# Kernel optimization log

Hardware: AMD Instinct MI355X
Metric: run time of the kernel (lower is better)

Reference implementation:

```python
import jax, jax.numpy as jnp
import numpy as np

B, S, NX, NH = 4, 1024, 1024, 16
HD = NX // NH  # head_features = 64


def setup_inputs() -> dict:
    key = jax.random.key(0)
    k1, k2, k3 = jax.random.split(key, 3)
    x = jax.random.normal(k1, (B, S, NX), dtype=jnp.float32)
    w_attn = 0.02 * jax.random.normal(k2, (NX, 3 * NX), dtype=jnp.float32)
    b_attn = jnp.zeros((3 * NX,), dtype=jnp.float32)
    w_proj = 0.02 * jax.random.normal(k3, (NX, NX), dtype=jnp.float32)
    b_proj = jnp.zeros((NX,), dtype=jnp.float32)
    causal_bias = jnp.tril(jnp.ones((S, S), dtype=jnp.float32))  # tril buffer
    return {"x": x, "w_attn": w_attn, "b_attn": b_attn,
            "w_proj": w_proj, "b_proj": b_proj, "causal_bias": causal_bias}


def reference(x, w_attn, b_attn, w_proj, b_proj, causal_bias):
    # c_attn: fused qkv projection (Conv1D == addmm)
    qkv = x @ w_attn + b_attn                     # [B, S, 3*NX]
    q, k, v = jnp.split(qkv, 3, axis=-1)          # each [B, S, NX]
    # split heads -> [B, H, S, D]
    q = q.reshape(B, S, NH, HD).transpose(0, 2, 1, 3)
    k = k.reshape(B, S, NH, HD).transpose(0, 2, 1, 3)
    v = v.reshape(B, S, NH, HD).transpose(0, 2, 1, 3)
    # present: stack of (key in [B,H,S,D] layout, value)
    present = jnp.stack((k, v))                   # [2, B, H, S, D]
    # scores with scale=True
    w = jnp.einsum('bhqd,bhkd->bhqk', q, k) / jnp.sqrt(jnp.float32(HD))
    b = causal_bias[None, None, :, :]             # [1,1,S,S] (nd==ns==S)
    w = w * b - 1e10 * (1.0 - b)                  # multiplicative mask trick
    p = jax.nn.softmax(w, axis=-1)
    a = jnp.einsum('bhqk,bhkd->bhqd', p, v)       # [B, H, S, D]
    a = a.transpose(0, 2, 1, 3).reshape(B, S, NX)  # merge heads
    out = a @ w_proj + b_proj                     # c_proj
    return out, present
```

## Files before the change

kernel.cpp:

```cpp
#include <hip/hip_runtime.h>
#include <hip/hip_bf16.h>

typedef __attribute__((ext_vector_type(8))) short short8;
typedef __attribute__((ext_vector_type(4))) float floatx4;

constexpr int Bsz = 4, Ssz = 1024, NXc = 1024, NHc = 16, HDc = 64;
constexpr int OUT_ELEMS  = Bsz * Ssz * NXc;
constexpr int HEAD_ELEMS = Bsz * NHc * Ssz * HDc;

union BF8 { __hip_bfloat16 h[8]; uint4 v; short8 s; };

__device__ __forceinline__ uint4 cvt8(const float* __restrict__ p) {
    float4 a = *reinterpret_cast<const float4*>(p);
    float4 b = *reinterpret_cast<const float4*>(p + 4);
    BF8 u;
    u.h[0] = __float2bfloat16(a.x); u.h[1] = __float2bfloat16(a.y);
    u.h[2] = __float2bfloat16(a.z); u.h[3] = __float2bfloat16(a.w);
    u.h[4] = __float2bfloat16(b.x); u.h[5] = __float2bfloat16(b.y);
    u.h[6] = __float2bfloat16(b.z); u.h[7] = __float2bfloat16(b.w);
    return u.v;
}

__device__ __forceinline__ void load_lds_16B(const void* g, void* l) {
    __builtin_amdgcn_global_load_lds(
        (const __attribute__((address_space(1))) unsigned int*)g,
        (__attribute__((address_space(3))) unsigned int*)l, 16, 0, 0);
}


__global__ __launch_bounds__(256) void cvt_kernel(
    const float* __restrict__ in, __hip_bfloat16* __restrict__ out, int n)
{
    int i = (blockIdx.x * 256 + threadIdx.x) * 8;
    if (i < n)
        *reinterpret_cast<uint4*>(out + i) = cvt8(in + i);
}

__global__ __launch_bounds__(256) void transpose_cvt(
    const float* __restrict__ in, __hip_bfloat16* __restrict__ out,
    int K, int N)
{
    __shared__ float t[64][65];
    const int tid = threadIdx.x;
    const int k0 = blockIdx.y * 64, n0 = blockIdx.x * 64;
#pragma unroll
    for (int j = 0; j < 16; ++j) {
        const int idx = tid + j * 256;
        const int row = idx >> 6, col = idx & 63;
        t[row][col] = in[(size_t)(k0 + row) * N + n0 + col];
    }
    __syncthreads();
#pragma unroll
    for (int j = 0; j < 16; ++j) {
        const int idx = tid + j * 256;
        const int orow = idx >> 6, ocol = idx & 63;
        out[(size_t)(n0 + orow) * K + k0 + ocol] = __float2bfloat16(t[ocol][orow]);
    }
}

__global__ __launch_bounds__(256) void vtrans(
    const float* __restrict__ vsrc, __hip_bfloat16* __restrict__ vtb)
{
    __shared__ float t[64][65];
    const int st = blockIdx.x, h = blockIdx.y, b = blockIdx.z;
    const int tid = threadIdx.x;
    const float* src = vsrc + ((size_t)((b * 16 + h) * Ssz + st * 64)) * HDc;
    __hip_bfloat16* dst = vtb + ((size_t)(b * 16 + h)) * (HDc * Ssz) + st * 64;
#pragma unroll
    for (int j = 0; j < 16; ++j) {
        const int idx = tid + j * 256;
        const int row = idx >> 6, col = idx & 63;
        t[row][col] = src[(size_t)row * 64 + col];
    }
    __syncthreads();
#pragma unroll
    for (int j = 0; j < 16; ++j) {
        const int idx = tid + j * 256;
        const int d = idx >> 6, s = idx & 63;
        dst[(size_t)d * Ssz + s] = __float2bfloat16(t[s][d]);
    }
}

template <int EPI>
__global__ __launch_bounds__(256) void gemm128(
    const __hip_bfloat16* __restrict__ A,
    const __hip_bfloat16* __restrict__ Bt,
    const float* __restrict__ bias,
    float* __restrict__ outf,
    __hip_bfloat16* __restrict__ qws,
    float* __restrict__ present,
    __hip_bfloat16* __restrict__ kbf,
    int M, int N, int K)
{
    __shared__ __align__(16) __hip_bfloat16 As[128 * 32];
    __shared__ __align__(16) __hip_bfloat16 Bs[128 * 32];

    const int tid  = threadIdx.x;
    const int w    = tid >> 6, lane = tid & 63;
    const int quad = lane >> 4, l16 = lane & 15;
    const int m0 = blockIdx.y * 128, n0 = blockIdx.x * 128;
    const int mb = (w >> 1) * 64, nbw = (w & 1) * 64;

    const int srow = lane >> 2;
    const int skseg = (lane & 3) * 8;

    floatx4 acc[4][4];
#pragma unroll
    for (int i = 0; i < 4; ++i)
#pragma unroll
        for (int j = 0; j < 4; ++j)
#pragma unroll
            for (int r = 0; r < 4; ++r) acc[i][j][r] = 0.f;

    for (int k0 = 0; k0 < K; k0 += 32) {
#pragma unroll
        for (int c = 0; c < 2; ++c) {
            const int chunk = w * 2 + c;
            const int row = chunk * 16 + srow;
            load_lds_16B(A + (size_t)(m0 + row) * K + k0 + skseg,
                         &As[chunk * 512]);
            load_lds_16B(Bt + (size_t)(n0 + row) * K + k0 + skseg,
                         &Bs[chunk * 512]);
        }
        __syncthreads();

        short8 af[4], bfr[4];
#pragma unroll
        for (int mi = 0; mi < 4; ++mi)
            af[mi] = *reinterpret_cast<const short8*>(
                &As[(mb + mi * 16 + l16) * 32 + quad * 8]);
#pragma unroll
        for (int ni = 0; ni < 4; ++ni)
            bfr[ni] = *reinterpret_cast<const short8*>(
                &Bs[(nbw + ni * 16 + l16) * 32 + quad * 8]);
#pragma unroll
        for (int mi = 0; mi < 4; ++mi)
#pragma unroll
            for (int ni = 0; ni < 4; ++ni)
                acc[mi][ni] = __builtin_amdgcn_mfma_f32_16x16x32_bf16(
                    af[mi], bfr[ni], acc[mi][ni], 0, 0, 0);

        __syncthreads();
    }

#pragma unroll
    for (int mi = 0; mi < 4; ++mi) {
#pragma unroll
        for (int ni = 0; ni < 4; ++ni) {
            const int col = n0 + nbw + ni * 16 + l16;
            const float bsv = bias[col];
#pragma unroll
            for (int r = 0; r < 4; ++r) {
                const int row = m0 + mb + mi * 16 + quad * 4 + r;
                const float v = acc[mi][ni][r] + bsv;
                if (EPI == 0) {
                    const int seg = col >> 10;
                    const int c = col & 1023;
                    if (seg == 0) {
                        qws[(size_t)row * 1024 + c] = __float2bfloat16(v);
                    } else {
                        const int b = row >> 10, s = row & 1023;
                        const int h = c >> 6, d = c & 63;
                        const size_t idx =
                            ((size_t)((b * 16 + h) * 1024 + s)) * 64 + d;
                        if (seg == 1) {
                            present[idx] = v;
                            kbf[idx] = __float2bfloat16(v);
                        } else {
                            present[HEAD_ELEMS + idx] = v;
                        }
                    }
                } else {
                    outf[(size_t)row * N + col] = v;
                }
            }
        }
    }
}

__global__ __launch_bounds__(256) void attn_v4(
    const __hip_bfloat16* __restrict__ qws,
    const __hip_bfloat16* __restrict__ kbf,
    const __hip_bfloat16* __restrict__ vtb,
    __hip_bfloat16* __restrict__ a_ws)
{
    const int bx = blockIdx.x, h = blockIdx.y, b = blockIdx.z;
    const int tid  = threadIdx.x;
    const int wave = tid >> 6, lane = tid & 63;
    const int quad = lane >> 4, l16 = lane & 15;
    const int stripe = wave * 16;

    __shared__ __align__(16) __hip_bfloat16 Ks[64 * 64];
    __shared__ __align__(16) __hip_bfloat16 Vts[64 * 64];
    __shared__ __align__(16) __hip_bfloat16 Ps[64][72];

    const __hip_bfloat16* Kbase = kbf + ((size_t)(b * 16 + h)) * (Ssz * HDc);
    const __hip_bfloat16* Vbase = vtb + ((size_t)(b * 16 + h)) * (HDc * Ssz);

    short8 ones;
#pragma unroll
    for (int i = 0; i < 8; ++i) ones[i] = (short)0x3F80;
    const float cexp = 0.18033688f;

#pragma unroll
    for (int pass = 0; pass < 2; ++pass) {
        const int qt = (pass == 0) ? (8 + bx) : (7 - bx);

        const __hip_bfloat16* Qb =
            qws + ((size_t)(b * Ssz + qt * 64 + stripe + l16)) * NXc + h * 64;
        short8 qf0 = *reinterpret_cast<const short8*>(Qb + quad * 8);
        short8 qf1 = *reinterpret_cast<const short8*>(Qb + 32 + quad * 8);

        floatx4 oacc[4], lacc;
#pragma unroll
        for (int ni = 0; ni < 4; ++ni)
#pragma unroll
            for (int r = 0; r < 4; ++r) oacc[ni][r] = 0.f;
#pragma unroll
        for (int r = 0; r < 4; ++r) lacc[r] = 0.f;

        for (int kt = 0; kt <= qt; ++kt) {
#pragma unroll
            for (int it = 0; it < 2; ++it) {
                const int slot = it * 256 + wave * 64 + lane;
                const int row = slot >> 3;
                const int p = (slot & 7) ^ (row & 7);
                load_lds_16B(
                    Kbase + (size_t)(kt * 64 + row) * 64 + p * 8,
                    &Ks[(size_t)(it * 256 + wave * 64) * 8]);
                load_lds_16B(
                    Vbase + (size_t)row * Ssz + kt * 64 + p * 8,
                    &Vts[(size_t)(it * 256 + wave * 64) * 8]);
            }
            __syncthreads();

            floatx4 sacc[4];
#pragma unroll
            for (int ni = 0; ni < 4; ++ni)
#pragma unroll
                for (int r = 0; r < 4; ++r) sacc[ni][r] = 0.f;
#pragma unroll
            for (int ni = 0; ni < 4; ++ni) {
                const int r = ni * 16 + l16;
                const int sw = r & 7;
                short8 kf0 = *reinterpret_cast<const short8*>(
                    &Ks[(r * 8 + (quad ^ sw)) * 8]);
                short8 kf1 = *reinterpret_cast<const short8*>(
                    &Ks[(r * 8 + ((4 + quad) ^ sw)) * 8]);
                sacc[ni] = __builtin_amdgcn_mfma_f32_16x16x32_bf16(
                    qf0, kf0, sacc[ni], 0, 0, 0);
                sacc[ni] = __builtin_amdgcn_mfma_f32_16x16x32_bf16(
                    qf1, kf1, sacc[ni], 0, 0, 0);
            }

            const bool diag = (kt == qt);
#pragma unroll
            for (int r = 0; r < 4; ++r) {
                const int lrow = stripe + quad * 4 + r;
#pragma unroll
                for (int nn = 0; nn < 4; ++nn) {
                    const int ni = (nn + quad) & 3;
                    const bool mask = diag && (ni * 16 + l16) > lrow;
                    const float p = mask ? 0.f : exp2f(sacc[ni][r] * cexp);
                    Ps[lrow][ni * 16 + l16] = __float2bfloat16(p);
                }
            }

#pragma unroll
            for (int kk = 0; kk < 64; kk += 32) {
                short8 pf = *reinterpret_cast<const short8*>(
                    &Ps[stripe + l16][kk + quad * 8]);
                lacc = __builtin_amdgcn_mfma_f32_16x16x32_bf16(
                    pf, ones, lacc, 0, 0, 0);
#pragma unroll
                for (int ni = 0; ni < 4; ++ni) {
                    const int r2 = ni * 16 + l16;
                    const int sw2 = r2 & 7;
                    short8 vf = *reinterpret_cast<const short8*>(
                        &Vts[(r2 * 8 + (((kk >> 3) + quad) ^ sw2)) * 8]);
                    oacc[ni] = __builtin_amdgcn_mfma_f32_16x16x32_bf16(
                        pf, vf, oacc[ni], 0, 0, 0);
                }
            }
            __syncthreads();
        }

#pragma unroll
        for (int r = 0; r < 4; ++r) {
            const float inv = 1.0f / fmaxf(lacc[r], 1e-20f);
            const int row = qt * 64 + stripe + quad * 4 + r;
#pragma unroll
            for (int ni = 0; ni < 4; ++ni) {
                const int col = h * 64 + ni * 16 + l16;
                a_ws[((size_t)(b * Ssz + row)) * NXc + col] =
                    __float2bfloat16(oacc[ni][r] * inv);
            }
        }
    }
}

__global__ __launch_bounds__(256) void attn_v3p(
    const __hip_bfloat16* __restrict__ qws,
    const float* __restrict__ present,
    __hip_bfloat16* __restrict__ a_ws)
{
    const int bx = blockIdx.x, h = blockIdx.y, b = blockIdx.z;
    const int tid  = threadIdx.x;
    const int wave = tid >> 6, lane = tid & 63;
    const int quad = lane >> 4, l16 = lane & 15;
    const int stripe = wave * 16;

    const size_t headoff = ((size_t)(b * 16 + h)) * Ssz * HDc;
    const float* Kp = present + headoff;
    const float* Vp = present + HEAD_ELEMS + headoff;

    __shared__ __align__(16) __hip_bfloat16 Ks[64][72];
    __shared__ __align__(16) __hip_bfloat16 Vts[64][72];
    __shared__ __align__(16) __hip_bfloat16 Ps[64][72];

    const int krow = tid >> 3, kseg = tid & 7;
    const int vd = tid & 63, vg = tid >> 6;

    short8 ones;
#pragma unroll
    for (int i = 0; i < 8; ++i) ones[i] = (short)0x3F80;
    const float cexp = 0.18033688f;

#pragma unroll
    for (int pass = 0; pass < 2; ++pass) {
        const int qt = (pass == 0) ? (8 + bx) : (7 - bx);

        const __hip_bfloat16* Qb =
            qws + ((size_t)(b * Ssz + qt * 64 + stripe + l16)) * NXc + h * 64;
        short8 qf0 = *reinterpret_cast<const short8*>(Qb + quad * 8);
        short8 qf1 = *reinterpret_cast<const short8*>(Qb + 32 + quad * 8);

        floatx4 oacc[4], lacc;
#pragma unroll
        for (int ni = 0; ni < 4; ++ni)
#pragma unroll
            for (int r = 0; r < 4; ++r) oacc[ni][r] = 0.f;
#pragma unroll
        for (int r = 0; r < 4; ++r) lacc[r] = 0.f;

        for (int kt = 0; kt <= qt; ++kt) {
#pragma unroll
            for (int it = 0; it < 2; ++it) {
                const int kr = krow + it * 32;
                *reinterpret_cast<uint4*>(&Ks[kr][kseg * 8]) =
                    cvt8(Kp + (size_t)(kt * 64 + kr) * 64 + kseg * 8);
                const int kb = (it * 4 + vg) * 8;
                BF8 u;
#pragma unroll
                for (int i = 0; i < 8; ++i)
                    u.h[i] = __float2bfloat16(
                        Vp[(size_t)(kt * 64 + kb + i) * 64 + vd]);
                *reinterpret_cast<uint4*>(&Vts[vd][kb]) = u.v;
            }
            __syncthreads();

            floatx4 sacc[4];
#pragma unroll
            for (int ni = 0; ni < 4; ++ni)
#pragma unroll
                for (int r = 0; r < 4; ++r) sacc[ni][r] = 0.f;
#pragma unroll
            for (int ni = 0; ni < 4; ++ni) {
                short8 kf0 = *reinterpret_cast<const short8*>(
                    &Ks[ni * 16 + l16][quad * 8]);
                short8 kf1 = *reinterpret_cast<const short8*>(
                    &Ks[ni * 16 + l16][32 + quad * 8]);
                sacc[ni] = __builtin_amdgcn_mfma_f32_16x16x32_bf16(
                    qf0, kf0, sacc[ni], 0, 0, 0);
                sacc[ni] = __builtin_amdgcn_mfma_f32_16x16x32_bf16(
                    qf1, kf1, sacc[ni], 0, 0, 0);
            }

            const bool diag = (kt == qt);
#pragma unroll
            for (int r = 0; r < 4; ++r) {
                const int lrow = stripe + quad * 4 + r;
#pragma unroll
                for (int nn = 0; nn < 4; ++nn) {
                    const int ni = (nn + quad) & 3;
                    const bool mask = diag && (ni * 16 + l16) > lrow;
                    const float p = mask ? 0.f : exp2f(sacc[ni][r] * cexp);
                    Ps[lrow][ni * 16 + l16] = __float2bfloat16(p);
                }
            }

#pragma unroll
            for (int kk = 0; kk < 64; kk += 32) {
                short8 pf = *reinterpret_cast<const short8*>(
                    &Ps[stripe + l16][kk + quad * 8]);
                lacc = __builtin_amdgcn_mfma_f32_16x16x32_bf16(
                    pf, ones, lacc, 0, 0, 0);
#pragma unroll
                for (int ni = 0; ni < 4; ++ni) {
                    short8 vf = *reinterpret_cast<const short8*>(
                        &Vts[ni * 16 + l16][kk + quad * 8]);
                    oacc[ni] = __builtin_amdgcn_mfma_f32_16x16x32_bf16(
                        pf, vf, oacc[ni], 0, 0, 0);
                }
            }
            __syncthreads();
        }

#pragma unroll
        for (int r = 0; r < 4; ++r) {
            const float inv = 1.0f / fmaxf(lacc[r], 1e-20f);
            const int row = qt * 64 + stripe + quad * 4 + r;
#pragma unroll
            for (int ni = 0; ni < 4; ++ni) {
                const int col = h * 64 + ni * 16 + l16;
                a_ws[((size_t)(b * Ssz + row)) * NXc + col] =
                    __float2bfloat16(oacc[ni][r] * inv);
            }
        }
    }
}

template <int EPI>
__global__ __launch_bounds__(256) void gemm64(
    const void* __restrict__ Av, const float* __restrict__ Bw,
    const float* __restrict__ bias, float* __restrict__ out0,
    float* __restrict__ present, int M, int N, int K)
{
    __shared__ __align__(16) __hip_bfloat16 As[64][40];
    __shared__ __align__(16) __hip_bfloat16 Bs[64][40];
    const int tid = threadIdx.x;
    const int wave = tid >> 6, lane = tid & 63;
    const int quad = lane >> 4, l16 = lane & 15;
    const int m0 = blockIdx.y * 64, n0 = blockIdx.x * 64;
    const int mb = (wave >> 1) * 32, nb = (wave & 1) * 32;
    const int arow = tid >> 2, aseg = tid & 3;
    const int brow = tid >> 3, bseg = tid & 7;
    floatx4 acc[2][2];
#pragma unroll
    for (int i = 0; i < 2; ++i)
#pragma unroll
        for (int j = 0; j < 2; ++j)
#pragma unroll
            for (int r = 0; r < 4; ++r) acc[i][j][r] = 0.f;
    for (int k0 = 0; k0 < K; k0 += 32) {
        if (EPI == 0) {
            const float* A = (const float*)Av;
            *reinterpret_cast<uint4*>(&As[arow][aseg * 8]) =
                cvt8(A + (size_t)(m0 + arow) * K + k0 + aseg * 8);
        } else {
            const __hip_bfloat16* A = (const __hip_bfloat16*)Av;
            *reinterpret_cast<uint4*>(&As[arow][aseg * 8]) =
                *reinterpret_cast<const uint4*>(
                    A + (size_t)(m0 + arow) * K + k0 + aseg * 8);
        }
        const float* bp = Bw + (size_t)(k0 + brow) * N + n0 + bseg * 8;
        float4 b0 = *reinterpret_cast<const float4*>(bp);
        float4 b1 = *reinterpret_cast<const float4*>(bp + 4);
        Bs[bseg * 8 + 0][brow] = __float2bfloat16(b0.x);
        Bs[bseg * 8 + 1][brow] = __float2bfloat16(b0.y);
        Bs[bseg * 8 + 2][brow] = __float2bfloat16(b0.z);
        Bs[bseg * 8 + 3][brow] = __float2bfloat16(b0.w);
        Bs[bseg * 8 + 4][brow] = __float2bfloat16(b1.x);
        Bs[bseg * 8 + 5][brow] = __float2bfloat16(b1.y);
        Bs[bseg * 8 + 6][brow] = __float2bfloat16(b1.z);
        Bs[bseg * 8 + 7][brow] = __float2bfloat16(b1.w);
        __syncthreads();
        short8 af[2], bf[2];
#pragma unroll
        for (int mm = 0; mm < 2; ++mm)
            af[mm] = *reinterpret_cast<const short8*>(&As[mb + mm * 16 + l16][quad * 8]);
#pragma unroll
        for (int nn = 0; nn < 2; ++nn)
            bf[nn] = *reinterpret_cast<const short8*>(&Bs[nb + nn * 16 + l16][quad * 8]);
#pragma unroll
        for (int mm = 0; mm < 2; ++mm)
#pragma unroll
            for (int nn = 0; nn < 2; ++nn)
                acc[mm][nn] = __builtin_amdgcn_mfma_f32_16x16x32_bf16(
                    af[mm], bf[nn], acc[mm][nn], 0, 0, 0);
        __syncthreads();
    }
#pragma unroll
    for (int mm = 0; mm < 2; ++mm)
#pragma unroll
        for (int nn = 0; nn < 2; ++nn) {
            const int col = n0 + nb + nn * 16 + l16;
            const float bsv = bias[col];
#pragma unroll
            for (int r = 0; r < 4; ++r) {
                const int row = m0 + mb + mm * 16 + quad * 4 + r;
                const float v = acc[mm][nn][r] + bsv;
                if (EPI == 0) {
                    const int seg = col >> 10;
                    const int c = col & 1023;
                    if (seg == 0) out0[(size_t)row * 1024 + c] = v;
                    else {
                        const int b = row >> 10, s = row & 1023;
                        const int h = c >> 6, d = c & 63;
                        const size_t idx = ((size_t)((b * 16 + h) * 1024 + s)) * 64 + d;
                        if (seg == 1) present[idx] = v;
                        else          present[HEAD_ELEMS + idx] = v;
                    }
                } else out0[(size_t)row * N + col] = v;
            }
        }
}

__global__ __launch_bounds__(256) void attn64(
    const float* __restrict__ qbuf, const float* __restrict__ present,
    __hip_bfloat16* __restrict__ a_ws)
{
    const int qt = blockIdx.x, h = blockIdx.y, b = blockIdx.z;
    const int tid = threadIdx.x;
    const int wave = tid >> 6, lane = tid & 63;
    const int quad = lane >> 4, l16 = lane & 15;
    const int mb = (wave >> 1) * 32, nb = (wave & 1) * 32;
    const size_t headoff = ((size_t)(b * 16 + h)) * Ssz * HDc;
    const float* Qb = qbuf + ((size_t)(b * Ssz + qt * 64)) * NXc + h * 64;
    const float* Kp = present + headoff;
    const float* Vp = present + HEAD_ELEMS + headoff;
    __shared__ __align__(16) __hip_bfloat16 Qs[64][72];
    __shared__ __align__(16) __hip_bfloat16 Ks[64][72];
    __shared__ __align__(16) __hip_bfloat16 Vts[64][72];
    __shared__ __align__(16) __hip_bfloat16 Ps[64][72];
    __shared__ float Sc[64][65];
    __shared__ float mrow[64], lrow[64], arw[64];
#pragma unroll
    for (int it = 0; it < 2; ++it) {
        const int c = tid + it * 256;
        const int row = c >> 3, seg = c & 7;
        *reinterpret_cast<uint4*>(&Qs[row][seg * 8]) =
            cvt8(Qb + (size_t)row * NXc + seg * 8);
    }
    if (tid < 64) { mrow[tid] = -1e9f; lrow[tid] = 0.f; }
    floatx4 oacc[2][2];
#pragma unroll
    for (int i = 0; i < 2; ++i)
#pragma unroll
        for (int j = 0; j < 2; ++j)
#pragma unroll
            for (int r = 0; r < 4; ++r) oacc[i][j][r] = 0.f;
    __syncthreads();
    for (int kt = 0; kt <= qt; ++kt) {
#pragma unroll
        for (int it = 0; it < 2; ++it) {
            const int c = tid + it * 256;
            const int row = c >> 3, seg = c & 7;
            *reinterpret_cast<uint4*>(&Ks[row][seg * 8]) =
                cvt8(Kp + (size_t)(kt * 64 + row) * 64 + seg * 8);
            const float* vp = Vp + (size_t)(kt * 64 + row) * 64 + seg * 8;
            float4 v0 = *reinterpret_cast<const float4*>(vp);
            float4 v1 = *reinterpret_cast<const float4*>(vp + 4);
            Vts[seg * 8 + 0][row] = __float2bfloat16(v0.x);
            Vts[seg * 8 + 1][row] = __float2bfloat16(v0.y);
            Vts[seg * 8 + 2][row] = __float2bfloat16(v0.z);
            Vts[seg * 8 + 3][row] = __float2bfloat16(v0.w);
            Vts[seg * 8 + 4][row] = __float2bfloat16(v1.x);
            Vts[seg * 8 + 5][row] = __float2bfloat16(v1.y);
            Vts[seg * 8 + 6][row] = __float2bfloat16(v1.z);
            Vts[seg * 8 + 7][row] = __float2bfloat16(v1.w);
        }
        __syncthreads();
        floatx4 sacc[2][2];
#pragma unroll
        for (int i = 0; i < 2; ++i)
#pragma unroll
            for (int j = 0; j < 2; ++j)
#pragma unroll
                for (int r = 0; r < 4; ++r) sacc[i][j][r] = 0.f;
#pragma unroll
        for (int kd = 0; kd < 64; kd += 32) {
            short8 af[2], bf[2];
#pragma unroll
            for (int mm = 0; mm < 2; ++mm)
                af[mm] = *reinterpret_cast<const short8*>(&Qs[mb + mm * 16 + l16][kd + quad * 8]);
#pragma unroll
            for (int nn = 0; nn < 2; ++nn)
                bf[nn] = *reinterpret_cast<const short8*>(&Ks[nb + nn * 16 + l16][kd + quad * 8]);
#pragma unroll
            for (int mm = 0; mm < 2; ++mm)
#pragma unroll
                for (int nn = 0; nn < 2; ++nn)
                    sacc[mm][nn] = __builtin_amdgcn_mfma_f32_16x16x32_bf16(
                        af[mm], bf[nn], sacc[mm][nn], 0, 0, 0);
        }
        const bool diag = (kt == qt);
#pragma unroll
        for (int mm = 0; mm < 2; ++mm)
#pragma unroll
            for (int nn = 0; nn < 2; ++nn)
#pragma unroll
                for (int r = 0; r < 4; ++r) {
                    const int row = mb + mm * 16 + quad * 4 + r;
                    const int col = nb + nn * 16 + l16;
                    float v = fminf(fmaxf(sacc[mm][nn][r] * 0.125f, -1e8f), 1e8f);
                    if (diag && col > row) v = -1e9f;
                    Sc[row][col] = v;
                }
        __syncthreads();
        if (tid < 64) {
            const int r = tid;
            const float mo = mrow[r];
            float mx = mo;
            for (int c = 0; c < 64; ++c) mx = fmaxf(mx, Sc[r][c]);
            const float al = (mo <= -5e8f) ? 0.f : __expf(mo - mx);
            float sum = 0.f;
            for (int c = 0; c < 64; ++c) {
                const float sv = Sc[r][c];
                const float p = (sv <= -5e8f) ? 0.f : __expf(sv - mx);
                sum += p;
                Ps[r][c] = __float2bfloat16(p);
            }
            mrow[r] = mx;
            lrow[r] = lrow[r] * al + sum;
            arw[r]  = al;
        }
        __syncthreads();
#pragma unroll
        for (int mm = 0; mm < 2; ++mm) {
            const int rbase = mb + mm * 16 + quad * 4;
#pragma unroll
            for (int r = 0; r < 4; ++r) {
                const float al = arw[rbase + r];
                oacc[mm][0][r] *= al;
                oacc[mm][1][r] *= al;
            }
        }
#pragma unroll
        for (int kk = 0; kk < 64; kk += 32) {
            short8 pf[2], vf[2];
#pragma unroll
            for (int mm = 0; mm < 2; ++mm)
                pf[mm] = *reinterpret_cast<const short8*>(&Ps[mb + mm * 16 + l16][kk + quad * 8]);
#pragma unroll
            for (int nn = 0; nn < 2; ++nn)
                vf[nn] = *reinterpret_cast<const short8*>(&Vts[nb + nn * 16 + l16][kk + quad * 8]);
#pragma unroll
            for (int mm = 0; mm < 2; ++mm)
#pragma unroll
                for (int nn = 0; nn < 2; ++nn)
                    oacc[mm][nn] = __builtin_amdgcn_mfma_f32_16x16x32_bf16(
                        pf[mm], vf[nn], oacc[mm][nn], 0, 0, 0);
        }
        __syncthreads();
    }
#pragma unroll
    for (int mm = 0; mm < 2; ++mm)
#pragma unroll
        for (int nn = 0; nn < 2; ++nn)
#pragma unroll
            for (int r = 0; r < 4; ++r) {
                const int row = mb + mm * 16 + quad * 4 + r;
                const int col = nb + nn * 16 + l16;
                const float inv = 1.0f / fmaxf(lrow[row], 1e-20f);
                a_ws[((size_t)(b * Ssz + qt * 64 + row)) * NXc + h * 64 + col] =
                    __float2bfloat16(oacc[mm][nn][r] * inv);
            }
}

extern "C" void kernel_launch(void* const* d_in, const int* in_sizes, int n_in,
                              void* d_out, int out_size, void* d_ws, size_t ws_size,
                              hipStream_t stream) {
    const float* x      = (const float*)d_in[0];
    const float* w_attn = (const float*)d_in[1];
    const float* b_attn = (const float*)d_in[2];
    const float* w_proj = (const float*)d_in[3];
    const float* b_proj = (const float*)d_in[4];

    float* out     = (float*)d_out;
    float* present = out + OUT_ELEMS;

    const size_t NEED_V4 = 40u * 1024u * 1024u;
    const size_t NEED_V3 = 32u * 1024u * 1024u;

    if (ws_size >= NEED_V4) {
        __hip_bfloat16* x_bf = (__hip_bfloat16*)d_ws;
        __hip_bfloat16* wTa  = x_bf + 4194304;
        __hip_bfloat16* wTp  = wTa + 3145728;
        __hip_bfloat16* q_ws = wTp + 1048576;
        __hip_bfloat16* k_bf = q_ws + 4194304;
        __hip_bfloat16* vT   = k_bf + 4194304;
        __hip_bfloat16* a_ws = x_bf;

        cvt_kernel<<<2048, 256, 0, stream>>>(x, x_bf, OUT_ELEMS);
        transpose_cvt<<<dim3(48, 16), 256, 0, stream>>>(w_attn, wTa, 1024, 3072);
        transpose_cvt<<<dim3(16, 16), 256, 0, stream>>>(w_proj, wTp, 1024, 1024);

        gemm128<0><<<dim3(24, 32), 256, 0, stream>>>(
            x_bf, wTa, b_attn, nullptr, q_ws, present, k_bf, 4096, 3072, 1024);

        vtrans<<<dim3(16, 16, 4), 256, 0, stream>>>(present + HEAD_ELEMS, vT);

        attn_v4<<<dim3(8, 16, 4), 256, 0, stream>>>(q_ws, k_bf, vT, a_ws);

        gemm128<1><<<dim3(8, 32), 256, 0, stream>>>(
            a_ws, wTp, b_proj, out, nullptr, nullptr, nullptr, 4096, 1024, 1024);
    } else if (ws_size >= NEED_V3) {
        __hip_bfloat16* a_ws = (__hip_bfloat16*)d_ws;
        __hip_bfloat16* q_ws = a_ws + 4194304;
        __hip_bfloat16* x_bf = q_ws + 4194304;
        __hip_bfloat16* wTa  = x_bf + 4194304;
        __hip_bfloat16* wTp  = wTa + 3145728;

        cvt_kernel<<<2048, 256, 0, stream>>>(x, x_bf, OUT_ELEMS);
        transpose_cvt<<<dim3(48, 16), 256, 0, stream>>>(w_attn, wTa, 1024, 3072);
        transpose_cvt<<<dim3(16, 16), 256, 0, stream>>>(w_proj, wTp, 1024, 1024);

        gemm128<0><<<dim3(24, 32), 256, 0, stream>>>(
            x_bf, wTa, b_attn, nullptr, q_ws, present, nullptr, 4096, 3072, 1024);

        attn_v3p<<<dim3(8, 16, 4), 256, 0, stream>>>(q_ws, present, a_ws);

        gemm128<1><<<dim3(8, 32), 256, 0, stream>>>(
            a_ws, wTp, b_proj, out, nullptr, nullptr, nullptr, 4096, 1024, 1024);
    } else {
        __hip_bfloat16* a_ws = (__hip_bfloat16*)d_ws;
        hipMemsetAsync(d_ws, 0, (size_t)OUT_ELEMS * sizeof(__hip_bfloat16), stream);
        gemm64<0><<<dim3(48, 64), 256, 0, stream>>>(x, w_attn, b_attn, out, present,
                                                    4096, 3072, 1024);
        attn64<<<dim3(16, 16, 4), 256, 0, stream>>>(out, present, a_ws);
        gemm64<1><<<dim3(16, 64), 256, 0, stream>>>(a_ws, w_proj, b_proj, out, nullptr,
                                                    4096, 1024, 1024);
    }
}
```

Before: 232.3 us.

## Swap GEMM operand roles for vectorized epilogue stores; flatten attention grid

The GEMMs now put the transposed weight in the MFMA A operand and the activations in B. Each lane then holds four consecutive output columns, so the bias loads and the fp32/bf16 epilogue stores become float4/uint2 vector writes instead of scalar strided ones. The attention kernel stops processing two paired query tiles per block and instead launches 1024 blocks, one per query tile. The tiles are ordered so that alternating batches reverse the tile order to spread causal work across blocks. The risk is load imbalance, because each block now has uneven causal work rather than paired work.

```diff
diff --git a/kernel.cpp b/kernel.cpp
--- a/kernel.cpp
+++ b/kernel.cpp
@@ -9,6 +9,7 @@
 constexpr int HEAD_ELEMS = Bsz * NHc * Ssz * HDc;
 
 union BF8 { __hip_bfloat16 h[8]; uint4 v; short8 s; };
+union BF4 { __hip_bfloat16 h[4]; uint2 v; };
 
 __device__ __forceinline__ uint4 cvt8(const float* __restrict__ p) {
     float4 a = *reinterpret_cast<const float4*>(p);
@@ -82,23 +83,24 @@
 }
 
 template <int EPI>
-__global__ __launch_bounds__(256) void gemm128(
-    const __hip_bfloat16* __restrict__ A,
-    const __hip_bfloat16* __restrict__ Bt,
+__global__ __launch_bounds__(256) void gemm128T(
+    const __hip_bfloat16* __restrict__ Wt,
+    const __hip_bfloat16* __restrict__ X,
     const float* __restrict__ bias,
     float* __restrict__ outf,
     __hip_bfloat16* __restrict__ qws,
     float* __restrict__ present,
     __hip_bfloat16* __restrict__ kbf,
-    int M, int N, int K)
+    int Nw, int Mx, int K)
 {
-    __shared__ __align__(16) __hip_bfloat16 As[128 * 32];
-    __shared__ __align__(16) __hip_bfloat16 Bs[128 * 32];
+    __shared__ __align__(16) __hip_bfloat16 Ws[128 * 32];
+    __shared__ __align__(16) __hip_bfloat16 Xs[128 * 32];
 
     const int tid  = threadIdx.x;
     const int w    = tid >> 6, lane = tid & 63;
     const int quad = lane >> 4, l16 = lane & 15;
-    const int m0 = blockIdx.y * 128, n0 = blockIdx.x * 128;
+    const int m0 = blockIdx.y * 128;
+    const int n0 = blockIdx.x * 128;
     const int mb = (w >> 1) * 64, nbw = (w & 1) * 64;
 
     const int srow = lane >> 2;
@@ -117,74 +119,85 @@
         for (int c = 0; c < 2; ++c) {
             const int chunk = w * 2 + c;
             const int row = chunk * 16 + srow;
-            load_lds_16B(A + (size_t)(m0 + row) * K + k0 + skseg,
-                         &As[chunk * 512]);
-            load_lds_16B(Bt + (size_t)(n0 + row) * K + k0 + skseg,
-                         &Bs[chunk * 512]);
-        }
-        __syncthreads();
-
-        short8 af[4], bfr[4];
+            load_lds_16B(Wt + (size_t)(m0 + row) * K + k0 + skseg,
+                         &Ws[chunk * 512]);
+            load_lds_16B(X + (size_t)(n0 + row) * K + k0 + skseg,
+                         &Xs[chunk * 512]);
+        }
+        __syncthreads();
+
+        short8 wf[4], xf[4];
 #pragma unroll
         for (int mi = 0; mi < 4; ++mi)
-            af[mi] = *reinterpret_cast<const short8*>(
-                &As[(mb + mi * 16 + l16) * 32 + quad * 8]);
+            wf[mi] = *reinterpret_cast<const short8*>(
+                &Ws[(mb + mi * 16 + l16) * 32 + quad * 8]);
 #pragma unroll
         for (int ni = 0; ni < 4; ++ni)
-            bfr[ni] = *reinterpret_cast<const short8*>(
-                &Bs[(nbw + ni * 16 + l16) * 32 + quad * 8]);
+            xf[ni] = *reinterpret_cast<const short8*>(
+                &Xs[(nbw + ni * 16 + l16) * 32 + quad * 8]);
 #pragma unroll
         for (int mi = 0; mi < 4; ++mi)
 #pragma unroll
             for (int ni = 0; ni < 4; ++ni)
                 acc[mi][ni] = __builtin_amdgcn_mfma_f32_16x16x32_bf16(
-                    af[mi], bfr[ni], acc[mi][ni], 0, 0, 0);
+                    wf[mi], xf[ni], acc[mi][ni], 0, 0, 0);
 
         __syncthreads();
     }
 
 #pragma unroll
     for (int mi = 0; mi < 4; ++mi) {
+        const int wcol = m0 + mb + mi * 16 + quad * 4;
+        const float4 b4 = *reinterpret_cast<const float4*>(&bias[wcol]);
 #pragma unroll
         for (int ni = 0; ni < 4; ++ni) {
-            const int col = n0 + nbw + ni * 16 + l16;
-            const float bsv = bias[col];
-#pragma unroll
-            for (int r = 0; r < 4; ++r) {
-                const int row = m0 + mb + mi * 16 + quad * 4 + r;
-                const float v = acc[mi][ni][r] + bsv;
-                if (EPI == 0) {
-                    const int seg = col >> 10;
-                    const int c = col & 1023;
-                    if (seg == 0) {
-                        qws[(size_t)row * 1024 + c] = __float2bfloat16(v);
+            const int xrow = n0 + nbw + ni * 16 + l16;
+            float4 v4;
+            v4.x = acc[mi][ni][0] + b4.x;
+            v4.y = acc[mi][ni][1] + b4.y;
+            v4.z = acc[mi][ni][2] + b4.z;
+            v4.w = acc[mi][ni][3] + b4.w;
+            if (EPI == 1) {
+                *reinterpret_cast<float4*>(&outf[(size_t)xrow * Nw + wcol]) = v4;
+            } else {
+                const int seg = wcol >> 10;
+                const int c = wcol & 1023;
+                BF4 hb;
+                hb.h[0] = __float2bfloat16(v4.x);
+                hb.h[1] = __float2bfloat16(v4.y);
+                hb.h[2] = __float2bfloat16(v4.z);
+                hb.h[3] = __float2bfloat16(v4.w);
+                if (seg == 0) {
+                    *reinterpret_cast<uint2*>(&qws[(size_t)xrow * 1024 + c]) = hb.v;
+                } else {
+                    const int b = xrow >> 10, s = xrow & 1023;
+                    const int h = c >> 6, d = c & 63;
+                    const size_t idx =
+                        ((size_t)((b * 16 + h) * 1024 + s)) * 64 + d;
+                    if (seg == 1) {
+                        *reinterpret_cast<float4*>(&present[idx]) = v4;
+                        if (kbf)
+                            *reinterpret_cast<uint2*>(&kbf[idx]) = hb.v;
                     } else {
-                        const int b = row >> 10, s = row & 1023;
-                        const int h = c >> 6, d = c & 63;
-                        const size_t idx =
-                            ((size_t)((b * 16 + h) * 1024 + s)) * 64 + d;
-                        if (seg == 1) {
-                            present[idx] = v;
-                            kbf[idx] = __float2bfloat16(v);
-                        } else {
-                            present[HEAD_ELEMS + idx] = v;
-                        }
+                        *reinterpret_cast<float4*>(&present[HEAD_ELEMS + idx]) = v4;
                     }
-                } else {
-                    outf[(size_t)row * N + col] = v;
                 }
             }
         }
     }
 }
 
-__global__ __launch_bounds__(256) void attn_v4(
+__global__ __launch_bounds__(256) void attn_v5(
     const __hip_bfloat16* __restrict__ qws,
     const __hip_bfloat16* __restrict__ kbf,
     const __hip_bfloat16* __restrict__ vtb,
     __hip_bfloat16* __restrict__ a_ws)
 {
-    const int bx = blockIdx.x, h = blockIdx.y, b = blockIdx.z;
+    const int i = blockIdx.x;
+    const int slot = i >> 8, u = i & 15, wq = (i >> 4) & 15;
+    const int qt = (slot & 1) ? (15 - u) : u;
+    const int h = wq, b = slot;
+
     const int tid  = threadIdx.x;
     const int wave = tid >> 6, lane = tid & 63;
     const int quad = lane >> 4, l16 = lane & 15;
@@ -199,102 +212,97 @@
 
     short8 ones;
 #pragma unroll
-    for (int i = 0; i < 8; ++i) ones[i] = (short)0x3F80;
+    for (int j = 0; j < 8; ++j) ones[j] = (short)0x3F80;
     const float cexp = 0.18033688f;
 
-#pragma unroll
-    for (int pass = 0; pass < 2; ++pass) {
-        const int qt = (pass == 0) ? (8 + bx) : (7 - bx);
-
-        const __hip_bfloat16* Qb =
-            qws + ((size_t)(b * Ssz + qt * 64 + stripe + l16)) * NXc + h * 64;
-        short8 qf0 = *reinterpret_cast<const short8*>(Qb + quad * 8);
-        short8 qf1 = *reinterpret_cast<const short8*>(Qb + 32 + quad * 8);
-
-        floatx4 oacc[4], lacc;
+    const __hip_bfloat16* Qb =
+        qws + ((size_t)(b * Ssz + qt * 64 + stripe + l16)) * NXc + h * 64;
+    short8 qf0 = *reinterpret_cast<const short8*>(Qb + quad * 8);
+    short8 qf1 = *reinterpret_cast<const short8*>(Qb + 32 + quad * 8);
+
+    floatx4 oacc[4], lacc;
+#pragma unroll
+    for (int ni = 0; ni < 4; ++ni)
+#pragma unroll
+        for (int r = 0; r < 4; ++r) oacc[ni][r] = 0.f;
+#pragma unroll
+    for (int r = 0; r < 4; ++r) lacc[r] = 0.f;
+
+    for (int kt = 0; kt <= qt; ++kt) {
+#pragma unroll
+        for (int it = 0; it < 2; ++it) {
+            const int slotg = it * 256 + wave * 64 + lane;
+            const int row = slotg >> 3;
+            const int p = (slotg & 7) ^ (row & 7);
+            load_lds_16B(
+                Kbase + (size_t)(kt * 64 + row) * 64 + p * 8,
+                &Ks[(size_t)(it * 256 + wave * 64) * 8]);
+            load_lds_16B(
+                Vbase + (size_t)row * Ssz + kt * 64 + p * 8,
+                &Vts[(size_t)(it * 256 + wave * 64) * 8]);
+        }
+        __syncthreads();
+
+        floatx4 sacc[4];
 #pragma unroll
         for (int ni = 0; ni < 4; ++ni)
 #pragma unroll
-            for (int r = 0; r < 4; ++r) oacc[ni][r] = 0.f;
-#pragma unroll
-        for (int r = 0; r < 4; ++r) lacc[r] = 0.f;
-
-        for (int kt = 0; kt <= qt; ++kt) {
-#pragma unroll
-            for (int it = 0; it < 2; ++it) {
-                const int slot = it * 256 + wave * 64 + lane;
-                const int row = slot >> 3;
-                const int p = (slot & 7) ^ (row & 7);
-                load_lds_16B(
-                    Kbase + (size_t)(kt * 64 + row) * 64 + p * 8,
-                    &Ks[(size_t)(it * 256 + wave * 64) * 8]);
-                load_lds_16B(
-                    Vbase + (size_t)row * Ssz + kt * 64 + p * 8,
-                    &Vts[(size_t)(it * 256 + wave * 64) * 8]);
-            }
-            __syncthreads();
-
-            floatx4 sacc[4];
-#pragma unroll
-            for (int ni = 0; ni < 4; ++ni)
-#pragma unroll
-                for (int r = 0; r < 4; ++r) sacc[ni][r] = 0.f;
+            for (int r = 0; r < 4; ++r) sacc[ni][r] = 0.f;
+#pragma unroll
+        for (int ni = 0; ni < 4; ++ni) {
+            const int r = ni * 16 + l16;
+            const int sw = r & 7;
+            short8 kf0 = *reinterpret_cast<const short8*>(
+                &Ks[(r * 8 + (quad ^ sw)) * 8]);
+            short8 kf1 = *reinterpret_cast<const short8*>(
+                &Ks[(r * 8 + ((4 + quad) ^ sw)) * 8]);
+            sacc[ni] = __builtin_amdgcn_mfma_f32_16x16x32_bf16(
+                qf0, kf0, sacc[ni], 0, 0, 0);
+            sacc[ni] = __builtin_amdgcn_mfma_f32_16x16x32_bf16(
+                qf1, kf1, sacc[ni], 0, 0, 0);
+        }
+
+        const bool diag = (kt == qt);
+#pragma unroll
+        for (int r = 0; r < 4; ++r) {
+            const int lrow = stripe + quad * 4 + r;
+#pragma unroll
+            for (int nn = 0; nn < 4; ++nn) {
+                const int ni = (nn + quad) & 3;
+                const bool mask = diag && (ni * 16 + l16) > lrow;
+                const float p = mask ? 0.f : exp2f(sacc[ni][r] * cexp);
+                Ps[lrow][ni * 16 + l16] = __float2bfloat16(p);
+            }
+        }
+
+#pragma unroll
+        for (int kk = 0; kk < 64; kk += 32) {
+            short8 pf = *reinterpret_cast<const short8*>(
+                &Ps[stripe + l16][kk + quad * 8]);
+            lacc = __builtin_amdgcn_mfma_f32_16x16x32_bf16(
+                pf, ones, lacc, 0, 0, 0);
 #pragma unroll
             for (int ni = 0; ni < 4; ++ni) {
-                const int r = ni * 16 + l16;
-                const int sw = r & 7;
-                short8 kf0 = *reinterpret_cast<const short8*>(
-                    &Ks[(r * 8 + (quad ^ sw)) * 8]);
-                short8 kf1 = *reinterpret_cast<const short8*>(
-                    &Ks[(r * 8 + ((4 + quad) ^ sw)) * 8]);
-                sacc[ni] = __builtin_amdgcn_mfma_f32_16x16x32_bf16(
-                    qf0, kf0, sacc[ni], 0, 0, 0);
-                sacc[ni] = __builtin_amdgcn_mfma_f32_16x16x32_bf16(
-                    qf1, kf1, sacc[ni], 0, 0, 0);
-            }
-
-            const bool diag = (kt == qt);
-#pragma unroll
-            for (int r = 0; r < 4; ++r) {
-                const int lrow = stripe + quad * 4 + r;
-#pragma unroll
-                for (int nn = 0; nn < 4; ++nn) {
-                    const int ni = (nn + quad) & 3;
-                    const bool mask = diag && (ni * 16 + l16) > lrow;
-                    const float p = mask ? 0.f : exp2f(sacc[ni][r] * cexp);
-                    Ps[lrow][ni * 16 + l16] = __float2bfloat16(p);
-                }
-            }
-
-#pragma unroll
-            for (int kk = 0; kk < 64; kk += 32) {
-                short8 pf = *reinterpret_cast<const short8*>(
-                    &Ps[stripe + l16][kk + quad * 8]);
-                lacc = __builtin_amdgcn_mfma_f32_16x16x32_bf16(
-                    pf, ones, lacc, 0, 0, 0);
-#pragma unroll
-                for (int ni = 0; ni < 4; ++ni) {
-                    const int r2 = ni * 16 + l16;
-                    const int sw2 = r2 & 7;
-                    short8 vf = *reinterpret_cast<const short8*>(
-                        &Vts[(r2 * 8 + (((kk >> 3) + quad) ^ sw2)) * 8]);
-                    oacc[ni] = __builtin_amdgcn_mfma_f32_16x16x32_bf16(
-                        pf, vf, oacc[ni], 0, 0, 0);
-                }
-            }
-            __syncthreads();
-        }
-
-#pragma unroll
-        for (int r = 0; r < 4; ++r) {
-            const float inv = 1.0f / fmaxf(lacc[r], 1e-20f);
-            const int row = qt * 64 + stripe + quad * 4 + r;
-#pragma unroll
-            for (int ni = 0; ni < 4; ++ni) {
-                const int col = h * 64 + ni * 16 + l16;
-                a_ws[((size_t)(b * Ssz + row)) * NXc + col] =
-                    __float2bfloat16(oacc[ni][r] * inv);
-            }
+                const int r2 = ni * 16 + l16;
+                const int sw2 = r2 & 7;
+                short8 vf = *reinterpret_cast<const short8*>(
+                    &Vts[(r2 * 8 + (((kk >> 3) + quad) ^ sw2)) * 8]);
+                oacc[ni] = __builtin_amdgcn_mfma_f32_16x16x32_bf16(
+                    pf, vf, oacc[ni], 0, 0, 0);
+            }
+        }
+        __syncthreads();
+    }
+
+#pragma unroll
+    for (int r = 0; r < 4; ++r) {
+        const float inv = 1.0f / fmaxf(lacc[r], 1e-20f);
+        const int row = qt * 64 + stripe + quad * 4 + r;
+#pragma unroll
+        for (int ni = 0; ni < 4; ++ni) {
+            const int col = h * 64 + ni * 16 + l16;
+            a_ws[((size_t)(b * Ssz + row)) * NXc + col] =
+                __float2bfloat16(oacc[ni][r] * inv);
         }
     }
 }
@@ -670,10 +678,10 @@
     float* out     = (float*)d_out;
     float* present = out + OUT_ELEMS;
 
-    const size_t NEED_V4 = 40u * 1024u * 1024u;
+    const size_t NEED_V5 = 40u * 1024u * 1024u;
     const size_t NEED_V3 = 32u * 1024u * 1024u;
 
-    if (ws_size >= NEED_V4) {
+    if (ws_size >= NEED_V5) {
         __hip_bfloat16* x_bf = (__hip_bfloat16*)d_ws;
         __hip_bfloat16* wTa  = x_bf + 4194304;
         __hip_bfloat16* wTp  = wTa + 3145728;
@@ -686,15 +694,15 @@
         transpose_cvt<<<dim3(48, 16), 256, 0, stream>>>(w_attn, wTa, 1024, 3072);
         transpose_cvt<<<dim3(16, 16), 256, 0, stream>>>(w_proj, wTp, 1024, 1024);
 
-        gemm128<0><<<dim3(24, 32), 256, 0, stream>>>(
-            x_bf, wTa, b_attn, nullptr, q_ws, present, k_bf, 4096, 3072, 1024);
+        gemm128T<0><<<dim3(32, 24), 256, 0, stream>>>(
+            wTa, x_bf, b_attn, nullptr, q_ws, present, k_bf, 3072, 4096, 1024);
 
         vtrans<<<dim3(16, 16, 4), 256, 0, stream>>>(present + HEAD_ELEMS, vT);
 
-        attn_v4<<<dim3(8, 16, 4), 256, 0, stream>>>(q_ws, k_bf, vT, a_ws);
-
-        gemm128<1><<<dim3(8, 32), 256, 0, stream>>>(
-            a_ws, wTp, b_proj, out, nullptr, nullptr, nullptr, 4096, 1024, 1024);
+        attn_v5<<<1024, 256, 0, stream>>>(q_ws, k_bf, vT, a_ws);
+
+        gemm128T<1><<<dim3(32, 8), 256, 0, stream>>>(
+            wTp, a_ws, b_proj, out, nullptr, nullptr, nullptr, 1024, 4096, 1024);
     } else if (ws_size >= NEED_V3) {
         __hip_bfloat16* a_ws = (__hip_bfloat16*)d_ws;
         __hip_bfloat16* q_ws = a_ws + 4194304;
@@ -706,13 +714,13 @@
         transpose_cvt<<<dim3(48, 16), 256, 0, stream>>>(w_attn, wTa, 1024, 3072);
         transpose_cvt<<<dim3(16, 16), 256, 0, stream>>>(w_proj, wTp, 1024, 1024);
 
-        gemm128<0><<<dim3(24, 32), 256, 0, stream>>>(
-            x_bf, wTa, b_attn, nullptr, q_ws, present, nullptr, 4096, 3072, 1024);
+        gemm128T<0><<<dim3(32, 24), 256, 0, stream>>>(
+            wTa, x_bf, b_attn, nullptr, q_ws, present, nullptr, 3072, 4096, 1024);
 
         attn_v3p<<<dim3(8, 16, 4), 256, 0, stream>>>(q_ws, present, a_ws);
 
-        gemm128<1><<<dim3(8, 32), 256, 0, stream>>>(
-            a_ws, wTp, b_proj, out, nullptr, nullptr, nullptr, 4096, 1024, 1024);
+        gemm128T<1><<<dim3(32, 8), 256, 0, stream>>>(
+            wTp, a_ws, b_proj, out, nullptr, nullptr, nullptr, 1024, 4096, 1024);
     } else {
         __hip_bfloat16* a_ws = (__hip_bfloat16*)d_ws;
         hipMemsetAsync(d_ws, 0, (size_t)OUT_ELEMS * sizeof(__hip_bfloat16), stream);
```

Result: slower. 248.3 us (+6.9%).
